# Optimization experiments

Hardware: AMD Instinct MI355X
Metric: run time of the kernel (lower is better)

Reference implementation:

```python
import jax, jax.numpy as jnp
import numpy as np

DIM = 512
BATCH, SEQ = 4, 4096


def setup_inputs() -> dict:
    key = jax.random.key(0)
    kx, kq, kk, kv, ko = jax.random.split(key, 5)
    s = DIM ** -0.5  # fan-in style init scale for stability
    return {
        "x": jax.random.normal(kx, (BATCH, SEQ, DIM), dtype=jnp.float32),
        "Wq": jax.random.normal(kq, (DIM, DIM), dtype=jnp.float32) * s,
        "Wk": jax.random.normal(kk, (DIM, DIM), dtype=jnp.float32) * s,
        "Wv": jax.random.normal(kv, (DIM, DIM), dtype=jnp.float32) * s,
        "Wo": jax.random.normal(ko, (DIM, DIM), dtype=jnp.float32) * s,
    }


def reference(x, Wq, Wk, Wv, Wo):
    # x: [B, S, D]; projections (torch Linear, no bias -> x @ W here)
    q = jnp.einsum('bsd,dk->bsk', x, Wq)  # [B,S,K]
    k = jnp.einsum('bsd,dk->bsk', x, Wk)  # [B,S,K]
    v = jnp.einsum('bsd,dv->bsv', x, Wv)  # [B,S,V]

    # sequential recurrence: M_t = M_{t-1} + v_t k_t^T ; y_t = M_t q_t
    def step(M, qkv_t):
        q_t, k_t, v_t = qkv_t  # each [B, K] / [B, V]
        M = M + v_t[:, :, None] * k_t[:, None, :]  # [B, V, K]
        y_t = jnp.einsum('bvk,bk->bv', M, q_t)
        return M, y_t

    M0 = jnp.zeros((x.shape[0], Wv.shape[1], Wk.shape[1]), dtype=x.dtype)
    qT = jnp.swapaxes(q, 0, 1)  # [S,B,K]
    kT = jnp.swapaxes(k, 0, 1)
    vT = jnp.swapaxes(v, 0, 1)
    _, ys = jax.lax.scan(step, M0, (qT, kT, vT))  # ys: [S,B,V]
    y = jnp.swapaxes(ys, 0, 1)  # [B,S,V]
    return jnp.einsum('bsv,vd->bsd', y, Wo)
```

## Files before the change

kernel.cpp:

```cpp
#include <hip/hip_runtime.h>
#include <hip/hip_bf16.h>

typedef __attribute__((ext_vector_type(8))) short bf16x8;
typedef __attribute__((ext_vector_type(4))) float f32x4;

__device__ inline short f2bf(float f) {
    __hip_bfloat16 h = __float2bfloat16(f);
    short s;
    __builtin_memcpy(&s, &h, 2);
    return s;
}
__device__ inline float bf2f(short s) {
    unsigned int u = ((unsigned int)(unsigned short)s) << 16;
    float f;
    __builtin_memcpy(&f, &u, 4);
    return f;
}

__device__ inline void cp16_async(const void* g, void* l) {
    __builtin_amdgcn_global_load_lds(
        (const __attribute__((address_space(1))) void*)g,
        (__attribute__((address_space(3))) void*)l, 16, 0, 0);
}


__global__ void prep_kernel(const float* __restrict__ x, short* __restrict__ Xb,
                            const float* __restrict__ W0, const float* __restrict__ W1,
                            const float* __restrict__ W2, const float* __restrict__ W3,
                            short* __restrict__ W4T) {
    int bid = blockIdx.x;
    if (bid < 8192) {
        int i = bid * 256 + threadIdx.x;
        float4 f = ((const float4*)x)[i];
        union { short s[4]; int2 v; } u;
        u.s[0] = f2bf(f.x); u.s[1] = f2bf(f.y); u.s[2] = f2bf(f.z); u.s[3] = f2bf(f.w);
        ((int2*)Xb)[i] = u.v;
    } else {
        int i = (bid - 8192) * 256 + threadIdx.x;
        int w = i >> 18;
        int r = i & 262143;
        int n = r >> 9, k = r & 511;
        const float* W = (w == 0) ? W0 : (w == 1) ? W1 : (w == 2) ? W2 : W3;
        W4T[i] = f2bf(W[k * 512 + n]);
    }
}


#define LDS_DECL __shared__ short sA0[4096], sA1[4096], sB0[4096], sB1[4096]

__device__ inline void mfma_kloop64(const short* __restrict__ A, int lda,
                                    const short* __restrict__ B, int ldb,
                                    int Kd, f32x4* acc,
                                    short* sA0, short* sA1, short* sB0, short* sB1) {
    const int tid = threadIdx.x, lane = tid & 63, wv = tid >> 6;
    const int quad = lane >> 4, lr = lane & 15;
    const int wr = (wv >> 1) * 64, wc = (wv & 1) * 64;
    const int c0 = tid, c1 = tid + 256;
    const int r0 = c0 >> 2, k80 = (c0 & 3) * 8;
    const int r1 = c1 >> 2, k81 = (c1 & 3) * 8;

    for (int k0 = 0; k0 < Kd; k0 += 64) {
        __syncthreads();
        cp16_async(A + (size_t)r0 * lda + k0 + k80,      sA0 + c0 * 8);
        cp16_async(A + (size_t)r1 * lda + k0 + k81,      sA0 + c1 * 8);
        cp16_async(A + (size_t)r0 * lda + k0 + 32 + k80, sA1 + c0 * 8);
        cp16_async(A + (size_t)r1 * lda + k0 + 32 + k81, sA1 + c1 * 8);
        cp16_async(B + (size_t)r0 * ldb + k0 + k80,      sB0 + c0 * 8);
        cp16_async(B + (size_t)r1 * ldb + k0 + k81,      sB0 + c1 * 8);
        cp16_async(B + (size_t)r0 * ldb + k0 + 32 + k80, sB1 + c0 * 8);
        cp16_async(B + (size_t)r1 * ldb + k0 + 32 + k81, sB1 + c1 * 8);
        __syncthreads();
#pragma unroll
        for (int half = 0; half < 2; ++half) {
            const short* pa = half ? sA1 : sA0;
            const short* pb = half ? sB1 : sB0;
            bf16x8 af[4], bfr[4];
#pragma unroll
            for (int i = 0; i < 4; ++i)
                af[i] = *(const bf16x8*)&pa[(wr + i * 16 + lr) * 32 + quad * 8];
#pragma unroll
            for (int j = 0; j < 4; ++j)
                bfr[j] = *(const bf16x8*)&pb[(wc + j * 16 + lr) * 32 + quad * 8];
#pragma unroll
            for (int i = 0; i < 4; ++i)
#pragma unroll
                for (int j = 0; j < 4; ++j)
                    acc[i * 4 + j] = __builtin_amdgcn_mfma_f32_16x16x32_bf16(af[i], bfr[j], acc[i * 4 + j], 0, 0, 0);
        }
    }
}

__device__ inline void store_out(float* p, float v) { *p = v; }
__device__ inline void store_out(short* p, float v) { *p = f2bf(v); }

template <typename OutT>
__device__ inline void store_tile128(OutT* C, int ldc, const f32x4* acc) {
    const int lane = threadIdx.x & 63, wv = threadIdx.x >> 6;
    const int quad = lane >> 4, lr = lane & 15;
    const int wr = (wv >> 1) * 64, wc = (wv & 1) * 64;
#pragma unroll
    for (int i = 0; i < 4; ++i)
#pragma unroll
        for (int j = 0; j < 4; ++j)
#pragma unroll
            for (int r = 0; r < 4; ++r)
                store_out(&C[(size_t)(wr + i * 16 + quad * 4 + r) * ldc + wc + j * 16 + lr],
                          acc[i * 4 + j][r]);
}

__global__ __launch_bounds__(256, 4) void proj_all(const short* __restrict__ Xb,
                                                   const short* __restrict__ W4T,
                                                   short* __restrict__ Qb, short* __restrict__ Kb,
                                                   short* __restrict__ Vt, short* __restrict__ Kt) {
    LDS_DECL;
    f32x4 acc[16];
#pragma unroll
    for (int i = 0; i < 16; ++i) acc[i] = (f32x4){0.f, 0.f, 0.f, 0.f};
    const int bid = blockIdx.x;
    const int lane = threadIdx.x & 63, wv = threadIdx.x >> 6;
    const int quad = lane >> 4, lr = lane & 15;
    const int wr = (wv >> 1) * 64, wc = (wv & 1) * 64;
    if (bid < 1024) {
        const int mt = bid >> 3, by = bid & 7;
        const short* At = Xb + (size_t)mt * 128 * 512;
        const short* Bt = W4T + (size_t)by * 128 * 512;
        short* Ct = ((by < 4) ? Qb : Kb) + (size_t)mt * 128 * 512 + (by & 3) * 128;
        mfma_kloop64(At, 512, Bt, 512, 512, acc, sA0, sA1, sB0, sB1);
        store_tile128(Ct, 512, acc);
        if (by >= 4) {
            const int b = mt >> 5;
            const int t0b = (mt & 31) * 128;
            const int f0 = (by - 4) * 128;
#pragma unroll
            for (int i = 0; i < 4; ++i)
#pragma unroll
                for (int j = 0; j < 4; ++j) {
                    int f = f0 + wc + j * 16 + lr;
                    int tt0 = t0b + wr + i * 16 + quad * 4;
                    short tmp[4];
#pragma unroll
                    for (int r = 0; r < 4; ++r) tmp[r] = f2bf(acc[i * 4 + j][r]);
                    *(int2*)&Kt[((size_t)b * 512 + f) * 4096 + tt0] = *(const int2*)tmp;
                }
        }
    } else {
        const int r = bid - 1024;
        const int b = r & 3, tt = (r >> 2) & 31, ft = r >> 7;
        const short* At = W4T + (size_t)2 * 262144 + (size_t)ft * 128 * 512;
        const short* Bt = Xb + ((size_t)b * 4096 + tt * 128) * 512;
        short* Ct = Vt + (size_t)b * 512 * 4096 + (size_t)ft * 128 * 4096 + tt * 128;
        mfma_kloop64(At, 512, Bt, 512, 512, acc, sA0, sA1, sB0, sB1);
        store_tile128(Ct, 4096, acc);
    }
}


__global__ __launch_bounds__(256, 4) void phaseA(const short* __restrict__ Vt,
                                                 const short* __restrict__ Kt,
                                                 short* __restrict__ AM) {
    LDS_DECL;
    const int bc = blockIdx.z, b = bc >> 4, c = bc & 15;
    const short* Ap = Vt + ((size_t)b * 512 + blockIdx.x * 128) * 4096 + c * 256;
    const short* Bp = Kt + ((size_t)b * 512 + blockIdx.y * 128) * 4096 + c * 256;
    short* Cp = AM + (size_t)bc * 262144 + (size_t)blockIdx.x * 128 * 512 + blockIdx.y * 128;
    f32x4 acc[16];
#pragma unroll
    for (int i = 0; i < 16; ++i) acc[i] = (f32x4){0.f, 0.f, 0.f, 0.f};
    mfma_kloop64(Ap, 4096, Bp, 4096, 256, acc, sA0, sA1, sB0, sB1);
    store_tile128(Cp, 512, acc);
}

__global__ __launch_bounds__(256, 4) void scan_phaseS(short* __restrict__ AM,
                                                      const short* __restrict__ Q,
                                                      const short* __restrict__ K,
                                                      short* __restrict__ P) {
    LDS_DECL;
    if (blockIdx.x < 512) {
        int i = blockIdx.x * 256 + threadIdx.x;
        int b = i >> 15;
        int vk8 = i & 32767;
        size_t base = (size_t)b * 16 * 262144 + (size_t)vk8 * 8;
        float acc[8];
#pragma unroll
        for (int s = 0; s < 8; ++s) acc[s] = 0.f;
        for (int c = 0; c < 16; ++c) {
            short* p = AM + base + (size_t)c * 262144;
            short in8[8];
            *(int4*)in8 = *(const int4*)p;
            short out8[8];
#pragma unroll
            for (int s = 0; s < 8; ++s) out8[s] = f2bf(acc[s]);
            *(int4*)p = *(const int4*)out8;
#pragma unroll
            for (int s = 0; s < 8; ++s) acc[s] += bf2f(in8[s]);
        }
        return;
    }
    const int e = blockIdx.x - 512;
    const int bc = e >> 2, mt = e & 1, nt = (e >> 1) & 1;
    if (mt < nt) return;
    const int b = bc >> 4, c = bc & 15;
    short* Pt = P + (size_t)bc * 65536 + (size_t)mt * 128 * 256 + nt * 128;
    const short* Ap = Q + ((size_t)(b * 4096 + c * 256 + mt * 128)) * 512;
    const short* Bp = K + ((size_t)(b * 4096 + c * 256 + nt * 128)) * 512;
    f32x4 acc[16];
#pragma unroll
    for (int i = 0; i < 16; ++i) acc[i] = (f32x4){0.f, 0.f, 0.f, 0.f};
    mfma_kloop64(Ap, 512, Bp, 512, 512, acc, sA0, sA1, sB0, sB1);
    const int lane = threadIdx.x & 63, wv = threadIdx.x >> 6;
    const int quad = lane >> 4, lr = lane & 15;
    const int wr = (wv >> 1) * 64, wc = (wv & 1) * 64;
    const bool diag = (mt == nt);
#pragma unroll
    for (int i = 0; i < 4; ++i)
#pragma unroll
        for (int j = 0; j < 4; ++j)
#pragma unroll
            for (int r = 0; r < 4; ++r) {
                int t = wr + i * 16 + quad * 4 + r;
                int jj = wc + j * 16 + lr;
                float v = (!diag || jj <= t) ? acc[i * 4 + j][r] : 0.f;
                Pt[(size_t)t * 256 + jj] = f2bf(v);
            }
}

__global__ __launch_bounds__(256, 4) void phaseY(const short* __restrict__ Q,
                                                 const short* __restrict__ Mpre,
                                                 const short* __restrict__ P,
                                                 const short* __restrict__ Vt,
                                                 short* __restrict__ Y) {
    LDS_DECL;
    const int bc = blockIdx.z, b = bc >> 4, c = bc & 15;
    const int mt = blockIdx.x, nt = blockIdx.y;
    f32x4 acc[16];
#pragma unroll
    for (int i = 0; i < 16; ++i) acc[i] = (f32x4){0.f, 0.f, 0.f, 0.f};
    const short* Ai = Q + ((size_t)(b * 4096 + c * 256 + mt * 128)) * 512;
    const short* Bi = Mpre + (size_t)bc * 262144 + (size_t)nt * 128 * 512;
    mfma_kloop64(Ai, 512, Bi, 512, 512, acc, sA0, sA1, sB0, sB1);
    const short* Ap = P + (size_t)bc * 65536 + (size_t)mt * 128 * 256;
    const short* Bv = Vt + ((size_t)b * 512 + nt * 128) * 4096 + c * 256;
    mfma_kloop64(Ap, 256, Bv, 4096, (mt + 1) * 128, acc, sA0, sA1, sB0, sB1);
    short* Cp = Y + ((size_t)(b * 4096 + c * 256 + mt * 128)) * 512 + nt * 128;
    store_tile128(Cp, 512, acc);
}

template <typename OutT>
__global__ __launch_bounds__(256, 4) void gemm128(const short* __restrict__ A, int lda,
                                                  const short* __restrict__ B, int ldb,
                                                  OutT* __restrict__ C, int ldc, int Kd) {
    LDS_DECL;
    const short* At = A + (size_t)blockIdx.x * 128 * lda;
    const short* Bt = B + (size_t)blockIdx.y * 128 * ldb;
    OutT* Ct = C + (size_t)blockIdx.x * 128 * ldc + blockIdx.y * 128;
    f32x4 acc[16];
#pragma unroll
    for (int i = 0; i < 16; ++i) acc[i] = (f32x4){0.f, 0.f, 0.f, 0.f};
    mfma_kloop64(At, lda, Bt, ldb, Kd, acc, sA0, sA1, sB0, sB1);
    store_tile128(Ct, ldc, acc);
}


extern "C" void kernel_launch(void* const* d_in, const int* in_sizes, int n_in,
                              void* d_out, int out_size, void* d_ws, size_t ws_size,
                              hipStream_t stream) {
    const float* x  = (const float*)d_in[0];
    const float* Wq = (const float*)d_in[1];
    const float* Wk = (const float*)d_in[2];
    const float* Wv = (const float*)d_in[3];
    const float* Wo = (const float*)d_in[4];
    float* out = (float*)d_out;

    const size_t NTD = 16384 * 512;

    short* ws  = (short*)d_ws;
    short* Xb  = ws;
    short* Qb  = Xb + NTD;
    short* Kb  = Qb + NTD;
    short* Kt  = Kb + NTD;
    short* Vt  = Kt + NTD;
    short* P   = Vt + NTD;
    short* W4T = P + 4194304;
    short* AM  = W4T + 1048576;
    short* Yb  = Kb;

    short* WoT = W4T + 3 * 262144;

    prep_kernel<<<12288, 256, 0, stream>>>(x, Xb, Wq, Wk, Wv, Wo, W4T);
    proj_all<<<1536, 256, 0, stream>>>(Xb, W4T, Qb, Kb, Vt, Kt);
    phaseA<<<dim3(4, 4, 64), 256, 0, stream>>>(Vt, Kt, AM);
    scan_phaseS<<<768, 256, 0, stream>>>(AM, Qb, Kb, P);
    phaseY<<<dim3(2, 4, 64), 256, 0, stream>>>(Qb, AM, P, Vt, Yb);
    gemm128<float><<<dim3(128, 4), 256, 0, stream>>>(Yb, 512, WoT, 512, out, 512, 512);
}
```

Measured before the change: 222.8 us.

## Double-buffer LDS tiles with XOR swizzle and prefetch next K tile during MFMA

Replaces the single-buffered GEMM K-loop with a two-stage pipeline: the next 64-wide K tile is loaded asynchronously into a second LDS buffer while MFMAs run on the current one, with a single barrier per iteration. The LDS layout moves to 64-element rows with an XOR swizzle to reduce bank conflicts on fragment reads. LDS use doubles to 64KB per block, so launch bounds drop from 4 to 2 blocks per CU, giving up occupancy in exchange for overlapping loads with compute.

```diff
diff --git a/kernel.cpp b/kernel.cpp
--- a/kernel.cpp
+++ b/kernel.cpp
@@ -46,47 +46,66 @@
 }
 
 
-#define LDS_DECL __shared__ short sA0[4096], sA1[4096], sB0[4096], sB1[4096]
-
-__device__ inline void mfma_kloop64(const short* __restrict__ A, int lda,
-                                    const short* __restrict__ B, int ldb,
-                                    int Kd, f32x4* acc,
-                                    short* sA0, short* sA1, short* sB0, short* sB1) {
+#define LDS_DECL __shared__ short sm[4][8192]
+
+__device__ inline void stage_tile(const short* __restrict__ A, int lda,
+                                  const short* __restrict__ B, int ldb, int k0,
+                                  short* sA, short* sB, int tid) {
+#pragma unroll
+    for (int j = 0; j < 4; ++j) {
+        const int L = tid * 16 + j * 4096;
+        const int row = L >> 7;
+        const int cb = (L & 127) ^ ((row & 7) << 4);
+        cp16_async(A + (size_t)row * lda + k0 + (cb >> 1), (char*)sA + L);
+        cp16_async(B + (size_t)row * ldb + k0 + (cb >> 1), (char*)sB + L);
+    }
+}
+
+__device__ inline void compute_tile(const short* sA, const short* sB, f32x4* acc,
+                                    int wr, int wc, int lr, int quad) {
+    const int sw = (lr & 7) << 3;
+#pragma unroll
+    for (int kk = 0; kk < 2; ++kk) {
+        const int co = (kk * 32 + quad * 8) ^ sw;
+        bf16x8 af[4], bfr[4];
+#pragma unroll
+        for (int i = 0; i < 4; ++i)
+            af[i] = *(const bf16x8*)&sA[(wr + i * 16 + lr) * 64 + co];
+#pragma unroll
+        for (int j = 0; j < 4; ++j)
+            bfr[j] = *(const bf16x8*)&sB[(wc + j * 16 + lr) * 64 + co];
+#pragma unroll
+        for (int i = 0; i < 4; ++i)
+#pragma unroll
+            for (int j = 0; j < 4; ++j)
+                acc[i * 4 + j] = __builtin_amdgcn_mfma_f32_16x16x32_bf16(af[i], bfr[j], acc[i * 4 + j], 0, 0, 0);
+    }
+}
+
+__device__ inline void kloop_pipe(const short* __restrict__ A, int lda,
+                                  const short* __restrict__ B, int ldb, int Kd,
+                                  f32x4* acc, short (*sm)[8192]) {
     const int tid = threadIdx.x, lane = tid & 63, wv = tid >> 6;
     const int quad = lane >> 4, lr = lane & 15;
     const int wr = (wv >> 1) * 64, wc = (wv & 1) * 64;
-    const int c0 = tid, c1 = tid + 256;
-    const int r0 = c0 >> 2, k80 = (c0 & 3) * 8;
-    const int r1 = c1 >> 2, k81 = (c1 & 3) * 8;
-
-    for (int k0 = 0; k0 < Kd; k0 += 64) {
-        __syncthreads();
-        cp16_async(A + (size_t)r0 * lda + k0 + k80,      sA0 + c0 * 8);
-        cp16_async(A + (size_t)r1 * lda + k0 + k81,      sA0 + c1 * 8);
-        cp16_async(A + (size_t)r0 * lda + k0 + 32 + k80, sA1 + c0 * 8);
-        cp16_async(A + (size_t)r1 * lda + k0 + 32 + k81, sA1 + c1 * 8);
-        cp16_async(B + (size_t)r0 * ldb + k0 + k80,      sB0 + c0 * 8);
-        cp16_async(B + (size_t)r1 * ldb + k0 + k81,      sB0 + c1 * 8);
-        cp16_async(B + (size_t)r0 * ldb + k0 + 32 + k80, sB1 + c0 * 8);
-        cp16_async(B + (size_t)r1 * ldb + k0 + 32 + k81, sB1 + c1 * 8);
-        __syncthreads();
-#pragma unroll
-        for (int half = 0; half < 2; ++half) {
-            const short* pa = half ? sA1 : sA0;
-            const short* pb = half ? sB1 : sB0;
-            bf16x8 af[4], bfr[4];
-#pragma unroll
-            for (int i = 0; i < 4; ++i)
-                af[i] = *(const bf16x8*)&pa[(wr + i * 16 + lr) * 32 + quad * 8];
-#pragma unroll
-            for (int j = 0; j < 4; ++j)
-                bfr[j] = *(const bf16x8*)&pb[(wc + j * 16 + lr) * 32 + quad * 8];
-#pragma unroll
-            for (int i = 0; i < 4; ++i)
-#pragma unroll
-                for (int j = 0; j < 4; ++j)
-                    acc[i * 4 + j] = __builtin_amdgcn_mfma_f32_16x16x32_bf16(af[i], bfr[j], acc[i * 4 + j], 0, 0, 0);
-        }
+    const int NT = Kd >> 6;
+    stage_tile(A, lda, B, ldb, 0, sm[0], sm[1], tid);
+    __builtin_amdgcn_sched_barrier(0);
+    asm volatile("s_waitcnt vmcnt(0)" ::: "memory");
+    __builtin_amdgcn_sched_barrier(0);
+    __builtin_amdgcn_s_barrier();
+    __builtin_amdgcn_sched_barrier(0);
+    for (int t = 0; t < NT; ++t) {
+        const int cur = (t & 1) << 1;
+        if (t + 1 < NT)
+            stage_tile(A, lda, B, ldb, (t + 1) << 6, sm[cur ^ 2], sm[cur ^ 3], tid);
+        __builtin_amdgcn_sched_barrier(0);
+        compute_tile(sm[cur], sm[cur + 1], acc, wr, wc, lr, quad);
+        __builtin_amdgcn_sched_barrier(0);
+        asm volatile("s_waitcnt vmcnt(0)" ::: "memory");
+        __builtin_amdgcn_sched_barrier(0);
+        __builtin_amdgcn_s_barrier();
+        __builtin_amdgcn_sched_barrier(0);
     }
 }
 
@@ -108,7 +127,7 @@
                           acc[i * 4 + j][r]);
 }
 
-__global__ __launch_bounds__(256, 4) void proj_all(const short* __restrict__ Xb,
+__global__ __launch_bounds__(256, 2) void proj_all(const short* __restrict__ Xb,
                                                    const short* __restrict__ W4T,
                                                    short* __restrict__ Qb, short* __restrict__ Kb,
                                                    short* __restrict__ Vt, short* __restrict__ Kt) {
@@ -125,7 +144,7 @@
         const short* At = Xb + (size_t)mt * 128 * 512;
         const short* Bt = W4T + (size_t)by * 128 * 512;
         short* Ct = ((by < 4) ? Qb : Kb) + (size_t)mt * 128 * 512 + (by & 3) * 128;
-        mfma_kloop64(At, 512, Bt, 512, 512, acc, sA0, sA1, sB0, sB1);
+        kloop_pipe(At, 512, Bt, 512, 512, acc, sm);
         store_tile128(Ct, 512, acc);
         if (by >= 4) {
             const int b = mt >> 5;
@@ -149,13 +168,13 @@
         const short* At = W4T + (size_t)2 * 262144 + (size_t)ft * 128 * 512;
         const short* Bt = Xb + ((size_t)b * 4096 + tt * 128) * 512;
         short* Ct = Vt + (size_t)b * 512 * 4096 + (size_t)ft * 128 * 4096 + tt * 128;
-        mfma_kloop64(At, 512, Bt, 512, 512, acc, sA0, sA1, sB0, sB1);
+        kloop_pipe(At, 512, Bt, 512, 512, acc, sm);
         store_tile128(Ct, 4096, acc);
     }
 }
 
 
-__global__ __launch_bounds__(256, 4) void phaseA(const short* __restrict__ Vt,
+__global__ __launch_bounds__(256, 2) void phaseA(const short* __restrict__ Vt,
                                                  const short* __restrict__ Kt,
                                                  short* __restrict__ AM) {
     LDS_DECL;
@@ -166,11 +185,11 @@
     f32x4 acc[16];
 #pragma unroll
     for (int i = 0; i < 16; ++i) acc[i] = (f32x4){0.f, 0.f, 0.f, 0.f};
-    mfma_kloop64(Ap, 4096, Bp, 4096, 256, acc, sA0, sA1, sB0, sB1);
+    kloop_pipe(Ap, 4096, Bp, 4096, 256, acc, sm);
     store_tile128(Cp, 512, acc);
 }
 
-__global__ __launch_bounds__(256, 4) void scan_phaseS(short* __restrict__ AM,
+__global__ __launch_bounds__(256, 2) void scan_phaseS(short* __restrict__ AM,
                                                       const short* __restrict__ Q,
                                                       const short* __restrict__ K,
                                                       short* __restrict__ P) {
@@ -206,7 +225,7 @@
     f32x4 acc[16];
 #pragma unroll
     for (int i = 0; i < 16; ++i) acc[i] = (f32x4){0.f, 0.f, 0.f, 0.f};
-    mfma_kloop64(Ap, 512, Bp, 512, 512, acc, sA0, sA1, sB0, sB1);
+    kloop_pipe(Ap, 512, Bp, 512, 512, acc, sm);
     const int lane = threadIdx.x & 63, wv = threadIdx.x >> 6;
     const int quad = lane >> 4, lr = lane & 15;
     const int wr = (wv >> 1) * 64, wc = (wv & 1) * 64;
@@ -224,7 +243,7 @@
             }
 }
 
-__global__ __launch_bounds__(256, 4) void phaseY(const short* __restrict__ Q,
+__global__ __launch_bounds__(256, 2) void phaseY(const short* __restrict__ Q,
                                                  const short* __restrict__ Mpre,
                                                  const short* __restrict__ P,
                                                  const short* __restrict__ Vt,
@@ -237,16 +256,16 @@
     for (int i = 0; i < 16; ++i) acc[i] = (f32x4){0.f, 0.f, 0.f, 0.f};
     const short* Ai = Q + ((size_t)(b * 4096 + c * 256 + mt * 128)) * 512;
     const short* Bi = Mpre + (size_t)bc * 262144 + (size_t)nt * 128 * 512;
-    mfma_kloop64(Ai, 512, Bi, 512, 512, acc, sA0, sA1, sB0, sB1);
+    kloop_pipe(Ai, 512, Bi, 512, 512, acc, sm);
     const short* Ap = P + (size_t)bc * 65536 + (size_t)mt * 128 * 256;
     const short* Bv = Vt + ((size_t)b * 512 + nt * 128) * 4096 + c * 256;
-    mfma_kloop64(Ap, 256, Bv, 4096, (mt + 1) * 128, acc, sA0, sA1, sB0, sB1);
+    kloop_pipe(Ap, 256, Bv, 4096, (mt + 1) * 128, acc, sm);
     short* Cp = Y + ((size_t)(b * 4096 + c * 256 + mt * 128)) * 512 + nt * 128;
     store_tile128(Cp, 512, acc);
 }
 
 template <typename OutT>
-__global__ __launch_bounds__(256, 4) void gemm128(const short* __restrict__ A, int lda,
+__global__ __launch_bounds__(256, 2) void gemm128(const short* __restrict__ A, int lda,
                                                   const short* __restrict__ B, int ldb,
                                                   OutT* __restrict__ C, int ldc, int Kd) {
     LDS_DECL;
@@ -256,7 +275,7 @@
     f32x4 acc[16];
 #pragma unroll
     for (int i = 0; i < 16; ++i) acc[i] = (f32x4){0.f, 0.f, 0.f, 0.f};
-    mfma_kloop64(At, lda, Bt, ldb, Kd, acc, sA0, sA1, sB0, sB1);
+    kloop_pipe(At, lda, Bt, ldb, Kd, acc, sm);
     store_tile128(Ct, ldc, acc);
 }
 
```

Measured after the change: 224.1 us. Within noise of the previous version (+0.6%).
